# Optimization experiments

Measured on AMD Instinct MI355X. Metric: run time of the kernel, lower is better.

Reference implementation:

```python
import jax, jax.numpy as jnp
import numpy as np

N, E, D, H, C, K = 50000, 800000, 64, 16, 40, 2


def setup_inputs() -> dict:
    key = jax.random.key(0)
    ks = jax.random.split(key, 6)
    x = jax.random.normal(ks[0], (N, D), dtype=jnp.float32)
    edge_index = jax.random.randint(ks[1], (2, E), 0, N, dtype=jnp.int32)
    W1 = jax.random.normal(ks[2], (K, D, H), dtype=jnp.float32) * 0.1
    b1 = jax.random.normal(ks[3], (H,), dtype=jnp.float32) * 0.1
    W2 = jax.random.normal(ks[4], (K, H, C), dtype=jnp.float32) * 0.1
    b2 = jax.random.normal(ks[5], (C,), dtype=jnp.float32) * 0.1
    return {"x": x, "edge_index": edge_index, "W1": W1, "b1": b1, "W2": W2, "b2": b2}


def _cheb_conv(x, src, dst, norm, W, b):
    # PyG ChebConv, K=2, sym norm, lambda_max=2:
    # scaled Laplacian L_hat = -D^{-1/2} A D^{-1/2}  (diag cancels to 0)
    # out = Tx0 @ W[0] + Tx1 @ W[1] + b,  Tx0 = x,  Tx1 = L_hat x
    n = x.shape[0]
    msgs = norm[:, None] * x[src]                      # [E, F] gather
    Tx1 = jax.ops.segment_sum(msgs, dst, num_segments=n)  # scatter-add
    return x @ W[0] + Tx1 @ W[1] + b


def reference(x, edge_index, W1, b1, W2, b2):
    src, dst = edge_index[0], edge_index[1]
    n = x.shape[0]
    # symmetric normalization coefficients (edge weights = 1)
    deg = jax.ops.segment_sum(jnp.ones((src.shape[0],), x.dtype), src, num_segments=n)
    dinv = jnp.where(deg > 0, jax.lax.rsqrt(jnp.maximum(deg, 1.0)), 0.0)
    norm = -dinv[src] * dinv[dst]
    h = jax.nn.relu(_cheb_conv(x, src, dst, norm, W1, b1))
    # dropout is identity in eval mode
    out = _cheb_conv(h, src, dst, norm, W2, b2)
    return jax.nn.log_softmax(out, axis=1)
```

## Files before the change

### kernel.cpp

```cpp
#include <hip/hip_runtime.h>
#include <math.h>

#define N_NODES 50000
#define N_EDGES 800000
#define D_IN    64
#define H_HID   16
#define C_OUT   40

#define BSH     7
#define BNODES  128
#define BMASK   127
#define NBUCK   ((N_NODES + BNODES - 1) / BNODES)
#define NBUCKP  400
#define NBLK    500
#define EPB     (N_EDGES / NBLK)
#define EPB4    (EPB / 4)

__global__ void bucket_count(const int* __restrict__ src, const int* __restrict__ dst,
                             int* __restrict__ partS, int* __restrict__ partD) {
    __shared__ int hS[NBUCK], hD[NBUCK];
    for (int i = threadIdx.x; i < NBUCK; i += blockDim.x) { hS[i] = 0; hD[i] = 0; }
    __syncthreads();
    const int4* s4 = (const int4*)(src + blockIdx.x * EPB);
    const int4* d4 = (const int4*)(dst + blockIdx.x * EPB);
    for (int k = threadIdx.x; k < EPB4; k += blockDim.x) {
        int4 s = s4[k], d = d4[k];
        atomicAdd(&hS[s.x >> BSH], 1); atomicAdd(&hS[s.y >> BSH], 1);
        atomicAdd(&hS[s.z >> BSH], 1); atomicAdd(&hS[s.w >> BSH], 1);
        atomicAdd(&hD[d.x >> BSH], 1); atomicAdd(&hD[d.y >> BSH], 1);
        atomicAdd(&hD[d.z >> BSH], 1); atomicAdd(&hD[d.w >> BSH], 1);
    }
    __syncthreads();
    for (int i = threadIdx.x; i < NBUCK; i += blockDim.x) {
        partS[blockIdx.x * NBUCKP + i] = hS[i];
        partD[blockIdx.x * NBUCKP + i] = hD[i];
    }
}

__global__ void bucket_base_scan(int* __restrict__ partS, int* __restrict__ partD,
                                 int* __restrict__ totS, int* __restrict__ totD) {
    int* part = blockIdx.y ? partD : partS;
    int* tot  = blockIdx.y ? totD  : totS;
    int b = blockIdx.x;
    __shared__ int s[512];
    int k = threadIdx.x;
    int v = (k < NBLK) ? part[k * NBUCKP + b] : 0;
    s[k] = v;
    __syncthreads();
    for (int off = 1; off < 512; off <<= 1) {
        int t = (k >= off) ? s[k - off] : 0;
        __syncthreads();
        s[k] += t;
        __syncthreads();
    }
    if (k < NBLK) part[k * NBUCKP + b] = s[k] - v;
    if (k == 511) tot[b] = s[511];
}

__global__ void bucket_base_final(const int* __restrict__ totS, const int* __restrict__ totD,
                                  int* __restrict__ baseS, int* __restrict__ baseD) {
    const int* tot = blockIdx.x ? totD : totS;
    int* base = blockIdx.x ? baseD : baseS;
    __shared__ int s[512];
    int k = threadIdx.x;
    int v = (k < NBUCK) ? tot[k] : 0;
    s[k] = v;
    __syncthreads();
    for (int off = 1; off < 512; off <<= 1) {
        int t = (k >= off) ? s[k - off] : 0;
        __syncthreads();
        s[k] += t;
        __syncthreads();
    }
    if (k < NBUCK) base[k] = s[k] - v;
    if (k == NBUCK - 1) base[NBUCK] = s[k];
}

__global__ void bucket_scatter(const int* __restrict__ src, const int* __restrict__ dst,
                               const int* __restrict__ partS, const int* __restrict__ partD,
                               const int* __restrict__ baseS, const int* __restrict__ baseD,
                               unsigned int* __restrict__ packedD,
                               unsigned char* __restrict__ srcloc) {
    __shared__ int cS[NBUCK], cD[NBUCK];
    int blk = blockIdx.x;
    for (int b = threadIdx.x; b < NBUCK; b += blockDim.x) {
        cS[b] = baseS[b] + partS[blk * NBUCKP + b];
        cD[b] = baseD[b] + partD[blk * NBUCKP + b];
    }
    __syncthreads();
    const int4* s4 = (const int4*)(src + blk * EPB);
    const int4* d4 = (const int4*)(dst + blk * EPB);
    for (int k = threadIdx.x; k < EPB4; k += blockDim.x) {
        int4 sv = s4[k], dv = d4[k];
        int ss[4] = { sv.x, sv.y, sv.z, sv.w };
        int dd[4] = { dv.x, dv.y, dv.z, dv.w };
        #pragma unroll
        for (int u = 0; u < 4; ++u) {
            int s = ss[u], d = dd[u];
            int pD = atomicAdd(&cD[d >> BSH], 1);
            packedD[pD] = (unsigned)s | ((unsigned)(d & BMASK) << 16);
            int pS = atomicAdd(&cS[s >> BSH], 1);
            srcloc[pS] = (unsigned char)(s & BMASK);
        }
    }
}

__global__ void csr_build(const unsigned int* __restrict__ packedD, const int* __restrict__ baseD,
                          const unsigned char* __restrict__ srcloc, const int* __restrict__ baseS,
                          int* __restrict__ col, int* __restrict__ rowptr,
                          float* __restrict__ dinv) {
    __shared__ int hist[BNODES], scanv[BNODES], cur[BNODES], shist[BNODES];
    int tid = threadIdx.x;
    if (tid < BNODES) { hist[tid] = 0; shist[tid] = 0; }
    __syncthreads();
    int bb = blockIdx.x;
    int begD = baseD[bb], endD = baseD[bb + 1];
    for (int j = begD + tid; j < endD; j += blockDim.x)
        atomicAdd(&hist[(packedD[j] >> 16) & BMASK], 1);
    int begS = baseS[bb], endS = baseS[bb + 1];
    for (int j = begS + tid; j < endS; j += blockDim.x)
        atomicAdd(&shist[srcloc[j]], 1);
    __syncthreads();
    if (tid == 0) {
        int acc = 0;
        for (int i = 0; i < BNODES; ++i) { scanv[i] = acc; acc += hist[i]; }
    }
    __syncthreads();
    if (tid < BNODES) {
        cur[tid] = scanv[tid];
        int node = bb * BNODES + tid;
        if (node < N_NODES) {
            rowptr[node] = begD + scanv[tid];
            int d = shist[tid];
            dinv[node] = (d > 0) ? rsqrtf((float)d) : 0.0f;
        }
    }
    if (bb == NBUCK - 1 && tid == 0) rowptr[N_NODES] = endD;
    __syncthreads();
    for (int j = begD + tid; j < endD; j += blockDim.x) {
        unsigned rec = packedD[j];
        int dl = (rec >> 16) & BMASK;
        int pos = atomicAdd(&cur[dl], 1);
        col[begD + pos] = (int)(rec & 0xFFFF);
    }
}

__global__ void xw_kernel(const float* __restrict__ x, const float* __restrict__ W1,
                          const float* __restrict__ dinv,
                          float* __restrict__ xw0, float* __restrict__ sxw1) {
    __shared__ float sW[2 * D_IN * H_HID];
    __shared__ float sx[16 * 65];
    for (int i = threadIdx.x; i < 2 * D_IN * H_HID; i += 256) sW[i] = W1[i];
    int nbase = blockIdx.x * 16;
    for (int i = threadIdx.x; i < 16 * D_IN; i += 256) {
        int r = i >> 6, c = i & 63;
        sx[r * 65 + c] = x[(size_t)(nbase + r) * D_IN + c];
    }
    __syncthreads();
    int nl = threadIdx.x >> 4, f = threadIdx.x & 15;
    int node = nbase + nl;
    float a0 = 0.f, a1 = 0.f;
    #pragma unroll
    for (int d = 0; d < D_IN; ++d) {
        float xv = sx[nl * 65 + d];
        a0 += xv * sW[d * H_HID + f];
        a1 += xv * sW[D_IN * H_HID + d * H_HID + f];
    }
    int t = node * H_HID + f;
    xw0[t]  = a0;
    sxw1[t] = dinv[node] * a1;
}

__global__ void gather1(const int* __restrict__ rowptr, const int* __restrict__ col,
                        const float* __restrict__ dinv, const float* __restrict__ sxw1,
                        const float* __restrict__ xw0, const float* __restrict__ b1,
                        float* __restrict__ h, float* __restrict__ sh) {
    int grp = threadIdx.x >> 2;
    int f4  = threadIdx.x & 3;
    int node = blockIdx.x * 128 + grp;
    if (node >= N_NODES) return;
    int beg = rowptr[node], end = rowptr[node + 1];
    const float4* sx4 = (const float4*)sxw1;
    float4 a = make_float4(0.f, 0.f, 0.f, 0.f);
    int j = beg;
    for (; j + 8 <= end; j += 8) {
        int c0 = col[j],     c1 = col[j + 1], c2 = col[j + 2], c3 = col[j + 3];
        int c4 = col[j + 4], c5 = col[j + 5], c6 = col[j + 6], c7 = col[j + 7];
        float4 v0 = sx4[c0 * 4 + f4], v1 = sx4[c1 * 4 + f4];
        float4 v2 = sx4[c2 * 4 + f4], v3 = sx4[c3 * 4 + f4];
        float4 v4 = sx4[c4 * 4 + f4], v5 = sx4[c5 * 4 + f4];
        float4 v6 = sx4[c6 * 4 + f4], v7 = sx4[c7 * 4 + f4];
        a.x += ((v0.x + v1.x) + (v2.x + v3.x)) + ((v4.x + v5.x) + (v6.x + v7.x));
        a.y += ((v0.y + v1.y) + (v2.y + v3.y)) + ((v4.y + v5.y) + (v6.y + v7.y));
        a.z += ((v0.z + v1.z) + (v2.z + v3.z)) + ((v4.z + v5.z) + (v6.z + v7.z));
        a.w += ((v0.w + v1.w) + (v2.w + v3.w)) + ((v4.w + v5.w) + (v6.w + v7.w));
    }
    for (; j < end; ++j) {
        float4 v = sx4[col[j] * 4 + f4];
        a.x += v.x; a.y += v.y; a.z += v.z; a.w += v.w;
    }
    float di = dinv[node];
    float4 x0 = ((const float4*)xw0)[node * 4 + f4];
    float4 bb = ((const float4*)b1)[f4];
    float vx = fmaxf(x0.x - di * a.x + bb.x, 0.f);
    float vy = fmaxf(x0.y - di * a.y + bb.y, 0.f);
    float vz = fmaxf(x0.z - di * a.z + bb.z, 0.f);
    float vw = fmaxf(x0.w - di * a.w + bb.w, 0.f);
    ((float4*)h)[node * 4 + f4]  = make_float4(vx, vy, vz, vw);
    ((float4*)sh)[node * 4 + f4] = make_float4(di * vx, di * vy, di * vz, di * vw);
}

#define HROW 20
__global__ void gather2_out(const int* __restrict__ rowptr, const int* __restrict__ col,
                            const float* __restrict__ dinv, const float* __restrict__ sh,
                            const float* __restrict__ h, const float* __restrict__ W2,
                            const float* __restrict__ b2, float* __restrict__ out) {
    __shared__ float sW0[H_HID * C_OUT], sW1[H_HID * C_OUT], sb[C_OUT];
    __shared__ float hrow[128][HROW];
    __shared__ float trow[128][HROW];
    for (int i = threadIdx.x; i < H_HID * C_OUT; i += 512) {
        sW0[i] = W2[i];
        sW1[i] = W2[H_HID * C_OUT + i];
    }
    if (threadIdx.x < C_OUT) sb[threadIdx.x] = b2[threadIdx.x];

    int grp = threadIdx.x >> 2;
    int f4  = threadIdx.x & 3;
    int node = blockIdx.x * 128 + grp;
    bool active = node < N_NODES;
    int beg = 0, end = 0;
    float di = 0.f;
    if (active) { beg = rowptr[node]; end = rowptr[node + 1]; di = dinv[node]; }
    const float4* sh4 = (const float4*)sh;
    float4 a = make_float4(0.f, 0.f, 0.f, 0.f);
    int j = beg;
    for (; j + 8 <= end; j += 8) {
        int c0 = col[j],     c1 = col[j + 1], c2 = col[j + 2], c3 = col[j + 3];
        int c4 = col[j + 4], c5 = col[j + 5], c6 = col[j + 6], c7 = col[j + 7];
        float4 v0 = sh4[c0 * 4 + f4], v1 = sh4[c1 * 4 + f4];
        float4 v2 = sh4[c2 * 4 + f4], v3 = sh4[c3 * 4 + f4];
        float4 v4 = sh4[c4 * 4 + f4], v5 = sh4[c5 * 4 + f4];
        float4 v6 = sh4[c6 * 4 + f4], v7 = sh4[c7 * 4 + f4];
        a.x += ((v0.x + v1.x) + (v2.x + v3.x)) + ((v4.x + v5.x) + (v6.x + v7.x));
        a.y += ((v0.y + v1.y) + (v2.y + v3.y)) + ((v4.y + v5.y) + (v6.y + v7.y));
        a.z += ((v0.z + v1.z) + (v2.z + v3.z)) + ((v4.z + v5.z) + (v6.z + v7.z));
        a.w += ((v0.w + v1.w) + (v2.w + v3.w)) + ((v4.w + v5.w) + (v6.w + v7.w));
    }
    for (; j < end; ++j) {
        float4 v = sh4[col[j] * 4 + f4];
        a.x += v.x; a.y += v.y; a.z += v.z; a.w += v.w;
    }
    float4 hp = make_float4(0.f, 0.f, 0.f, 0.f);
    if (active) hp = ((const float4*)h)[node * 4 + f4];
    hrow[grp][4 * f4 + 0] = hp.x;
    hrow[grp][4 * f4 + 1] = hp.y;
    hrow[grp][4 * f4 + 2] = hp.z;
    hrow[grp][4 * f4 + 3] = hp.w;
    trow[grp][4 * f4 + 0] = -di * a.x;
    trow[grp][4 * f4 + 1] = -di * a.y;
    trow[grp][4 * f4 + 2] = -di * a.z;
    trow[grp][4 * f4 + 3] = -di * a.w;
    __syncthreads();

    float hv[H_HID], tv[H_HID];
    #pragma unroll
    for (int ff = 0; ff < H_HID; ++ff) {
        hv[ff] = hrow[grp][ff];
        tv[ff] = trow[grp][ff];
    }
    float o[10];
    float mx = -1e30f;
    #pragma unroll
    for (int i = 0; i < 10; ++i) {
        int c = f4 * 10 + i;
        float aa = sb[c];
        #pragma unroll
        for (int ff = 0; ff < H_HID; ++ff)
            aa += hv[ff] * sW0[ff * C_OUT + c] + tv[ff] * sW1[ff * C_OUT + c];
        o[i] = aa;
        mx = fmaxf(mx, aa);
    }
    mx = fmaxf(mx, __shfl_xor(mx, 1));
    mx = fmaxf(mx, __shfl_xor(mx, 2));
    float sum = 0.f;
    #pragma unroll
    for (int i = 0; i < 10; ++i) sum += expf(o[i] - mx);
    sum += __shfl_xor(sum, 1);
    sum += __shfl_xor(sum, 2);
    float lse = mx + logf(sum);
    if (active) {
        float* op = out + (size_t)node * C_OUT + f4 * 10;
        #pragma unroll
        for (int i = 0; i < 10; ++i) op[i] = o[i] - lse;
    }
}

extern "C" void kernel_launch(void* const* d_in, const int* in_sizes, int n_in,
                              void* d_out, int out_size, void* d_ws, size_t ws_size,
                              hipStream_t stream) {
    const float* x   = (const float*)d_in[0];
    const int*   ei  = (const int*)d_in[1];
    const float* W1  = (const float*)d_in[2];
    const float* b1  = (const float*)d_in[3];
    const float* W2  = (const float*)d_in[4];
    const float* b2  = (const float*)d_in[5];
    float* out = (float*)d_out;

    const int* src = ei;
    const int* dst = ei + N_EDGES;

    int* partS = (int*)d_ws;
    int* partD = partS + NBLK * NBUCKP;
    int* baseS = partD + NBLK * NBUCKP;
    int* baseD = baseS + 512;
    int* totS  = baseD + 512;
    int* totD  = totS + 512;
    unsigned int*  packedD = (unsigned int*)(totD + 512);
    unsigned char* srcloc  = (unsigned char*)(packedD + N_EDGES);
    int*   col    = (int*)(srcloc + N_EDGES);
    int*   rowptr = col + N_EDGES;
    float* dinv   = (float*)(rowptr + N_NODES + 8);
    float* xw0    = dinv + N_NODES;
    float* sxw1   = xw0  + (size_t)N_NODES * H_HID;
    float* h      = sxw1 + (size_t)N_NODES * H_HID;
    float* sh     = h    + (size_t)N_NODES * H_HID;

    bucket_count    <<<NBLK, 256, 0, stream>>>(src, dst, partS, partD);
    bucket_base_scan<<<dim3(NBUCK, 2), 512, 0, stream>>>(partS, partD, totS, totD);
    bucket_base_final<<<2, 512, 0, stream>>>(totS, totD, baseS, baseD);
    bucket_scatter  <<<NBLK, 256, 0, stream>>>(src, dst, partS, partD, baseS, baseD, packedD, srcloc);
    csr_build       <<<NBUCK, 512, 0, stream>>>(packedD, baseD, srcloc, baseS, col, rowptr, dinv);
    xw_kernel       <<<N_NODES / 16, 256, 0, stream>>>(x, W1, dinv, xw0, sxw1);
    gather1         <<<(N_NODES + 127) / 128, 512, 0, stream>>>(rowptr, col, dinv, sxw1, xw0, b1, h, sh);
    gather2_out     <<<(N_NODES + 127) / 128, 512, 0, stream>>>(rowptr, col, dinv, sh, h, W2, b2, out);
}
```

Baseline: 90.35 us.

## Split neighbor gathers across two lane groups and fuse final bucket scan

Each node's neighbor list in gather1 and gather2_out is now walked by two 4-lane groups, taking alternating chunks of 8 edges, with the partial sums combined by a shuffle. This halves nodes per block and spreads the output softmax over 8 lanes, aiming to expose more memory-level parallelism per row. The separate bucket_base_final launch is folded into bucket_base_scan: the last block to finish, detected with an atomic counter, runs the final scan, which removes one kernel launch. Bucket width grows from 128 to 256 nodes, halving the bucket count. In exchange, lanes sit idle on short rows and the last-block pattern adds an atomic and a fence.

```diff
diff --git a/kernel.cpp b/kernel.cpp
--- a/kernel.cpp
+++ b/kernel.cpp
@@ -7,17 +7,19 @@
 #define H_HID   16
 #define C_OUT   40
 
-#define BSH     7
-#define BNODES  128
-#define BMASK   127
+#define BSH     8
+#define BNODES  256
+#define BMASK   255
 #define NBUCK   ((N_NODES + BNODES - 1) / BNODES)
-#define NBUCKP  400
+#define NBUCKP  200
 #define NBLK    500
 #define EPB     (N_EDGES / NBLK)
 #define EPB4    (EPB / 4)
 
 __global__ void bucket_count(const int* __restrict__ src, const int* __restrict__ dst,
-                             int* __restrict__ partS, int* __restrict__ partD) {
+                             int* __restrict__ partS, int* __restrict__ partD,
+                             unsigned int* __restrict__ done) {
+    if (blockIdx.x == 0 && threadIdx.x == 0) *done = 0;
     __shared__ int hS[NBUCK], hD[NBUCK];
     for (int i = threadIdx.x; i < NBUCK; i += blockDim.x) { hS[i] = 0; hD[i] = 0; }
     __syncthreads();
@@ -38,11 +40,14 @@
 }
 
 __global__ void bucket_base_scan(int* __restrict__ partS, int* __restrict__ partD,
-                                 int* __restrict__ totS, int* __restrict__ totD) {
+                                 int* __restrict__ totS, int* __restrict__ totD,
+                                 int* __restrict__ baseS, int* __restrict__ baseD,
+                                 unsigned int* __restrict__ done) {
     int* part = blockIdx.y ? partD : partS;
     int* tot  = blockIdx.y ? totD  : totS;
     int b = blockIdx.x;
     __shared__ int s[512];
+    __shared__ unsigned int rank;
     int k = threadIdx.x;
     int v = (k < NBLK) ? part[k * NBUCKP + b] : 0;
     s[k] = v;
@@ -55,25 +60,29 @@
     }
     if (k < NBLK) part[k * NBUCKP + b] = s[k] - v;
     if (k == 511) tot[b] = s[511];
-}
-
-__global__ void bucket_base_final(const int* __restrict__ totS, const int* __restrict__ totD,
-                                  int* __restrict__ baseS, int* __restrict__ baseD) {
-    const int* tot = blockIdx.x ? totD : totS;
-    int* base = blockIdx.x ? baseD : baseS;
-    __shared__ int s[512];
-    int k = threadIdx.x;
-    int v = (k < NBUCK) ? tot[k] : 0;
-    s[k] = v;
-    __syncthreads();
-    for (int off = 1; off < 512; off <<= 1) {
-        int t = (k >= off) ? s[k - off] : 0;
-        __syncthreads();
-        s[k] += t;
-        __syncthreads();
-    }
-    if (k < NBUCK) base[k] = s[k] - v;
-    if (k == NBUCK - 1) base[NBUCK] = s[k];
+    __threadfence();
+    __syncthreads();
+    if (k == 0) rank = atomicAdd(done, 1u);
+    __syncthreads();
+    if (rank == 2 * NBUCK - 1) {
+        for (int which = 0; which < 2; ++which) {
+            const int* t = which ? totD : totS;
+            int* base = which ? baseD : baseS;
+            int vv = (k < NBUCK) ? t[k] : 0;
+            __syncthreads();
+            s[k] = vv;
+            __syncthreads();
+            for (int off = 1; off < 512; off <<= 1) {
+                int tt = (k >= off) ? s[k - off] : 0;
+                __syncthreads();
+                s[k] += tt;
+                __syncthreads();
+            }
+            if (k < NBUCK) base[k] = s[k] - vv;
+            if (k == NBUCK - 1) base[NBUCK] = s[k];
+            __syncthreads();
+        }
+    }
 }
 
 __global__ void bucket_scatter(const int* __restrict__ src, const int* __restrict__ dst,
@@ -175,15 +184,16 @@
                         const float* __restrict__ dinv, const float* __restrict__ sxw1,
                         const float* __restrict__ xw0, const float* __restrict__ b1,
                         float* __restrict__ h, float* __restrict__ sh) {
-    int grp = threadIdx.x >> 2;
-    int f4  = threadIdx.x & 3;
-    int node = blockIdx.x * 128 + grp;
+    int grp  = threadIdx.x >> 2;
+    int f4   = threadIdx.x & 3;
+    int half = grp & 1;
+    int node = blockIdx.x * 64 + (grp >> 1);
     if (node >= N_NODES) return;
     int beg = rowptr[node], end = rowptr[node + 1];
     const float4* sx4 = (const float4*)sxw1;
     float4 a = make_float4(0.f, 0.f, 0.f, 0.f);
-    int j = beg;
-    for (; j + 8 <= end; j += 8) {
+    int j = beg + half * 8;
+    for (; j + 8 <= end; j += 16) {
         int c0 = col[j],     c1 = col[j + 1], c2 = col[j + 2], c3 = col[j + 3];
         int c4 = col[j + 4], c5 = col[j + 5], c6 = col[j + 6], c7 = col[j + 7];
         float4 v0 = sx4[c0 * 4 + f4], v1 = sx4[c1 * 4 + f4];
@@ -199,15 +209,21 @@
         float4 v = sx4[col[j] * 4 + f4];
         a.x += v.x; a.y += v.y; a.z += v.z; a.w += v.w;
     }
-    float di = dinv[node];
-    float4 x0 = ((const float4*)xw0)[node * 4 + f4];
-    float4 bb = ((const float4*)b1)[f4];
-    float vx = fmaxf(x0.x - di * a.x + bb.x, 0.f);
-    float vy = fmaxf(x0.y - di * a.y + bb.y, 0.f);
-    float vz = fmaxf(x0.z - di * a.z + bb.z, 0.f);
-    float vw = fmaxf(x0.w - di * a.w + bb.w, 0.f);
-    ((float4*)h)[node * 4 + f4]  = make_float4(vx, vy, vz, vw);
-    ((float4*)sh)[node * 4 + f4] = make_float4(di * vx, di * vy, di * vz, di * vw);
+    a.x += __shfl_xor(a.x, 4);
+    a.y += __shfl_xor(a.y, 4);
+    a.z += __shfl_xor(a.z, 4);
+    a.w += __shfl_xor(a.w, 4);
+    if (!half) {
+        float di = dinv[node];
+        float4 x0 = ((const float4*)xw0)[node * 4 + f4];
+        float4 bb = ((const float4*)b1)[f4];
+        float vx = fmaxf(x0.x - di * a.x + bb.x, 0.f);
+        float vy = fmaxf(x0.y - di * a.y + bb.y, 0.f);
+        float vz = fmaxf(x0.z - di * a.z + bb.z, 0.f);
+        float vw = fmaxf(x0.w - di * a.w + bb.w, 0.f);
+        ((float4*)h)[node * 4 + f4]  = make_float4(vx, vy, vz, vw);
+        ((float4*)sh)[node * 4 + f4] = make_float4(di * vx, di * vy, di * vz, di * vw);
+    }
 }
 
 #define HROW 20
@@ -216,25 +232,27 @@
                             const float* __restrict__ h, const float* __restrict__ W2,
                             const float* __restrict__ b2, float* __restrict__ out) {
     __shared__ float sW0[H_HID * C_OUT], sW1[H_HID * C_OUT], sb[C_OUT];
-    __shared__ float hrow[128][HROW];
-    __shared__ float trow[128][HROW];
+    __shared__ float hrow[64][HROW];
+    __shared__ float trow[64][HROW];
     for (int i = threadIdx.x; i < H_HID * C_OUT; i += 512) {
         sW0[i] = W2[i];
         sW1[i] = W2[H_HID * C_OUT + i];
     }
     if (threadIdx.x < C_OUT) sb[threadIdx.x] = b2[threadIdx.x];
 
-    int grp = threadIdx.x >> 2;
-    int f4  = threadIdx.x & 3;
-    int node = blockIdx.x * 128 + grp;
+    int grp  = threadIdx.x >> 2;
+    int f4   = threadIdx.x & 3;
+    int half = grp & 1;
+    int nl   = grp >> 1;
+    int node = blockIdx.x * 64 + nl;
     bool active = node < N_NODES;
     int beg = 0, end = 0;
     float di = 0.f;
     if (active) { beg = rowptr[node]; end = rowptr[node + 1]; di = dinv[node]; }
     const float4* sh4 = (const float4*)sh;
     float4 a = make_float4(0.f, 0.f, 0.f, 0.f);
-    int j = beg;
-    for (; j + 8 <= end; j += 8) {
+    int j = beg + half * 8;
+    for (; j + 8 <= end; j += 16) {
         int c0 = col[j],     c1 = col[j + 1], c2 = col[j + 2], c3 = col[j + 3];
         int c4 = col[j + 4], c5 = col[j + 5], c6 = col[j + 6], c7 = col[j + 7];
         float4 v0 = sh4[c0 * 4 + f4], v1 = sh4[c1 * 4 + f4];
@@ -250,29 +268,36 @@
         float4 v = sh4[col[j] * 4 + f4];
         a.x += v.x; a.y += v.y; a.z += v.z; a.w += v.w;
     }
-    float4 hp = make_float4(0.f, 0.f, 0.f, 0.f);
-    if (active) hp = ((const float4*)h)[node * 4 + f4];
-    hrow[grp][4 * f4 + 0] = hp.x;
-    hrow[grp][4 * f4 + 1] = hp.y;
-    hrow[grp][4 * f4 + 2] = hp.z;
-    hrow[grp][4 * f4 + 3] = hp.w;
-    trow[grp][4 * f4 + 0] = -di * a.x;
-    trow[grp][4 * f4 + 1] = -di * a.y;
-    trow[grp][4 * f4 + 2] = -di * a.z;
-    trow[grp][4 * f4 + 3] = -di * a.w;
-    __syncthreads();
-
+    a.x += __shfl_xor(a.x, 4);
+    a.y += __shfl_xor(a.y, 4);
+    a.z += __shfl_xor(a.z, 4);
+    a.w += __shfl_xor(a.w, 4);
+    if (!half) {
+        float4 hp = make_float4(0.f, 0.f, 0.f, 0.f);
+        if (active) hp = ((const float4*)h)[node * 4 + f4];
+        hrow[nl][4 * f4 + 0] = hp.x;
+        hrow[nl][4 * f4 + 1] = hp.y;
+        hrow[nl][4 * f4 + 2] = hp.z;
+        hrow[nl][4 * f4 + 3] = hp.w;
+        trow[nl][4 * f4 + 0] = -di * a.x;
+        trow[nl][4 * f4 + 1] = -di * a.y;
+        trow[nl][4 * f4 + 2] = -di * a.z;
+        trow[nl][4 * f4 + 3] = -di * a.w;
+    }
+    __syncthreads();
+
+    int l8 = threadIdx.x & 7;
     float hv[H_HID], tv[H_HID];
     #pragma unroll
     for (int ff = 0; ff < H_HID; ++ff) {
-        hv[ff] = hrow[grp][ff];
-        tv[ff] = trow[grp][ff];
-    }
-    float o[10];
+        hv[ff] = hrow[nl][ff];
+        tv[ff] = trow[nl][ff];
+    }
+    float o[5];
     float mx = -1e30f;
     #pragma unroll
-    for (int i = 0; i < 10; ++i) {
-        int c = f4 * 10 + i;
+    for (int i = 0; i < 5; ++i) {
+        int c = l8 * 5 + i;
         float aa = sb[c];
         #pragma unroll
         for (int ff = 0; ff < H_HID; ++ff)
@@ -282,16 +307,18 @@
     }
     mx = fmaxf(mx, __shfl_xor(mx, 1));
     mx = fmaxf(mx, __shfl_xor(mx, 2));
+    mx = fmaxf(mx, __shfl_xor(mx, 4));
     float sum = 0.f;
     #pragma unroll
-    for (int i = 0; i < 10; ++i) sum += expf(o[i] - mx);
+    for (int i = 0; i < 5; ++i) sum += expf(o[i] - mx);
     sum += __shfl_xor(sum, 1);
     sum += __shfl_xor(sum, 2);
+    sum += __shfl_xor(sum, 4);
     float lse = mx + logf(sum);
     if (active) {
-        float* op = out + (size_t)node * C_OUT + f4 * 10;
+        float* op = out + (size_t)node * C_OUT + l8 * 5;
         #pragma unroll
-        for (int i = 0; i < 10; ++i) op[i] = o[i] - lse;
+        for (int i = 0; i < 5; ++i) op[i] = o[i] - lse;
     }
 }
 
@@ -315,7 +342,8 @@
     int* baseD = baseS + 512;
     int* totS  = baseD + 512;
     int* totD  = totS + 512;
-    unsigned int*  packedD = (unsigned int*)(totD + 512);
+    unsigned int* done = (unsigned int*)(totD + 512);
+    unsigned int*  packedD = (unsigned int*)(done + 4);
     unsigned char* srcloc  = (unsigned char*)(packedD + N_EDGES);
     int*   col    = (int*)(srcloc + N_EDGES);
     int*   rowptr = col + N_EDGES;
@@ -325,12 +353,11 @@
     float* h      = sxw1 + (size_t)N_NODES * H_HID;
     float* sh     = h    + (size_t)N_NODES * H_HID;
 
-    bucket_count    <<<NBLK, 256, 0, stream>>>(src, dst, partS, partD);
-    bucket_base_scan<<<dim3(NBUCK, 2), 512, 0, stream>>>(partS, partD, totS, totD);
-    bucket_base_final<<<2, 512, 0, stream>>>(totS, totD, baseS, baseD);
+    bucket_count    <<<NBLK, 256, 0, stream>>>(src, dst, partS, partD, done);
+    bucket_base_scan<<<dim3(NBUCK, 2), 512, 0, stream>>>(partS, partD, totS, totD, baseS, baseD, done);
     bucket_scatter  <<<NBLK, 256, 0, stream>>>(src, dst, partS, partD, baseS, baseD, packedD, srcloc);
     csr_build       <<<NBUCK, 512, 0, stream>>>(packedD, baseD, srcloc, baseS, col, rowptr, dinv);
     xw_kernel       <<<N_NODES / 16, 256, 0, stream>>>(x, W1, dinv, xw0, sxw1);
-    gather1         <<<(N_NODES + 127) / 128, 512, 0, stream>>>(rowptr, col, dinv, sxw1, xw0, b1, h, sh);
-    gather2_out     <<<(N_NODES + 127) / 128, 512, 0, stream>>>(rowptr, col, dinv, sh, h, W2, b2, out);
-}
+    gather1         <<<(N_NODES + 63) / 64, 512, 0, stream>>>(rowptr, col, dinv, sxw1, xw0, b1, h, sh);
+    gather2_out     <<<(N_NODES + 63) / 64, 512, 0, stream>>>(rowptr, col, dinv, sh, h, W2, b2, out);
+}
```

After: 171.0 us. +89.2%, slower.
